# Kernel optimization log

Hardware: AMD Instinct MI355X
Metric: run time of the kernel (lower is better)

## Reference

```python
import jax, jax.numpy as jnp
import numpy as np

RADIUS = 5          # box-filter radius -> 11x11 kernel
TEMP = 0.5          # multinomial temperature
NSAMP = 5           # sampling_num
EPS = 1e-6
BN_EPS = 1e-5


def _conv(x, w, stride=1, padding=0, groups=1):
    return jax.lax.conv_general_dilated(
        x, w, window_strides=(stride, stride),
        padding=[(padding, padding), (padding, padding)],
        feature_group_count=groups,
        dimension_numbers=("NCHW", "OIHW", "NCHW"))


def custom_conv(x, w, key, stride=1, padding=0):
    """conv2d with cosine-activation regularization (bias=False path)."""
    B = x.shape[0]
    Cout = w.shape[0]
    # all-ones 'norm' conv on x*x
    x_norm = jnp.sqrt(_conv(x * x, jnp.ones_like(w), stride, padding))
    y = _conv(x, w, stride, padding)
    w_norm = jnp.sqrt(jnp.sum(w * w, axis=(1, 2, 3)))  # per-out-channel Frobenius norm
    cosine = y / (w_norm[None, :, None, None] + EPS) / (x_norm + EPS)
    # 11x11 depthwise box filter
    k = 2 * RADIUS + 1
    dw = jnp.ones((Cout, 1, k, k), x.dtype)
    cosine_mean = _conv(cosine, dw, 1, RADIUS, groups=Cout) / (k * k)
    H, W = cosine.shape[2], cosine.shape[3]
    # multinomial(NSAMP, exp(cosine/TEMP)) counts, no_grad in original
    logits = jax.lax.stop_gradient(cosine).reshape(B, Cout, H * W) / TEMP
    idx = jax.random.categorical(key, logits, axis=-1, shape=(NSAMP, B, Cout))
    bi = jnp.broadcast_to(jnp.arange(B)[None, :, None], (NSAMP, B, Cout))
    ci = jnp.broadcast_to(jnp.arange(Cout)[None, None, :], (NSAMP, B, Cout))
    mask = jnp.zeros((B, Cout, H * W), x.dtype).at[bi, ci, idx].add(1.0)
    cm = cosine_mean.reshape(B, Cout, H * W)
    act = ((mask * cm).sum(-1) / mask.sum(-1)).mean()
    return y, act


def batchnorm(x, g, b):
    # training-mode batch statistics (biased variance), like nn.BatchNorm2d
    m = x.mean(axis=(0, 2, 3), keepdims=True)
    v = x.var(axis=(0, 2, 3), keepdims=True)
    return (x - m) / jnp.sqrt(v + BN_EPS) * g[None, :, None, None] + b[None, :, None, None]


def setup_inputs() -> dict:
    key = jax.random.key(0)
    ks = jax.random.split(key, 10)
    x = jax.random.normal(ks[0], (16, 256, 56, 56), jnp.float32)
    w1 = jax.random.normal(ks[1], (64, 256, 1, 1), jnp.float32) * 0.05
    w2 = jax.random.normal(ks[2], (64, 64, 3, 3), jnp.float32) * 0.05
    w3 = jax.random.normal(ks[3], (256, 64, 1, 1), jnp.float32) * 0.05
    g1 = 1.0 + 0.05 * jax.random.normal(ks[4], (64,), jnp.float32)
    b1 = 0.05 * jax.random.normal(ks[5], (64,), jnp.float32)
    g2 = 1.0 + 0.05 * jax.random.normal(ks[6], (64,), jnp.float32)
    b2 = 0.05 * jax.random.normal(ks[7], (64,), jnp.float32)
    g3 = 1.0 + 0.05 * jax.random.normal(ks[8], (256,), jnp.float32)
    b3 = 0.05 * jax.random.normal(ks[9], (256,), jnp.float32)
    return {"x": x, "w1": w1, "w2": w2, "w3": w3,
            "g1": g1, "b1": b1, "g2": g2, "b2": b2, "g3": g3, "b3": b3}


def reference(x, w1, w2, w3, g1, b1, g2, b2, g3, b3):
    k0, k1, k2 = jax.random.split(jax.random.key(42), 3)
    acc = jnp.asarray(0.0, x.dtype)
    out, a = custom_conv(x, w1, k0)           # conv1x1
    acc = acc + a
    out = jax.nn.relu(batchnorm(out, g1, b1))
    out, a = custom_conv(out, w2, k1, padding=1)  # conv3x3, stride 1
    acc = acc + a
    out = jax.nn.relu(batchnorm(out, g2, b2))
    out, a = custom_conv(out, w3, k2)         # conv1x1 expand
    acc = acc + a
    out = batchnorm(out, g3, b3)
    out = jax.nn.relu(out + x)                # identity shortcut (downsample=None)
    return out, acc
```

## Files before the change

### kernel.cpp

```cpp
#include <hip/hip_runtime.h>
#include <stdint.h>
#include <math.h>

#define HW 3136
#define NPIX 50176

typedef __attribute__((ext_vector_type(8))) short bf16x8;
typedef __attribute__((ext_vector_type(4))) float f32x4;
#define MFMA16(a, b, c) __builtin_amdgcn_mfma_f32_16x16x32_bf16(a, b, c, 0, 0, 0)

__device__ __forceinline__ unsigned short f2bf(float f) {
  unsigned u = __float_as_uint(f);
  u = (u + 0x7fffu + ((u >> 16) & 1u)) >> 16;
  return (unsigned short)u;
}
__device__ __forceinline__ unsigned pk2(float a, float b) {
  return (unsigned)f2bf(a) | ((unsigned)f2bf(b) << 16);
}
__device__ __forceinline__ float bf2f(unsigned short h) {
  return __uint_as_float(((unsigned)h) << 16);
}

#define ROTL32(v, r) __builtin_rotateleft32((uint32_t)(v), (r))

__host__ __device__ inline void threefry2x32(uint32_t k0, uint32_t k1,
                                             uint32_t x0, uint32_t x1,
                                             uint32_t& o0, uint32_t& o1) {
  uint32_t k2 = k0 ^ k1 ^ 0x1BD11BDAu;
  x0 += k0; x1 += k1;
  x0 += x1; x1 = ROTL32(x1, 13); x1 ^= x0;
  x0 += x1; x1 = ROTL32(x1, 15); x1 ^= x0;
  x0 += x1; x1 = ROTL32(x1, 26); x1 ^= x0;
  x0 += x1; x1 = ROTL32(x1, 6);  x1 ^= x0;
  x0 += k1; x1 += k2 + 1u;
  x0 += x1; x1 = ROTL32(x1, 17); x1 ^= x0;
  x0 += x1; x1 = ROTL32(x1, 29); x1 ^= x0;
  x0 += x1; x1 = ROTL32(x1, 16); x1 ^= x0;
  x0 += x1; x1 = ROTL32(x1, 24); x1 ^= x0;
  x0 += k2; x1 += k0 + 2u;
  x0 += x1; x1 = ROTL32(x1, 13); x1 ^= x0;
  x0 += x1; x1 = ROTL32(x1, 15); x1 ^= x0;
  x0 += x1; x1 = ROTL32(x1, 26); x1 ^= x0;
  x0 += x1; x1 = ROTL32(x1, 6);  x1 ^= x0;
  x0 += k0; x1 += k1 + 3u;
  x0 += x1; x1 = ROTL32(x1, 17); x1 ^= x0;
  x0 += x1; x1 = ROTL32(x1, 29); x1 ^= x0;
  x0 += x1; x1 = ROTL32(x1, 16); x1 ^= x0;
  x0 += x1; x1 = ROTL32(x1, 24); x1 ^= x0;
  x0 += k1; x1 += k2 + 4u;
  x0 += x1; x1 = ROTL32(x1, 13); x1 ^= x0;
  x0 += x1; x1 = ROTL32(x1, 15); x1 ^= x0;
  x0 += x1; x1 = ROTL32(x1, 26); x1 ^= x0;
  x0 += x1; x1 = ROTL32(x1, 6);  x1 ^= x0;
  x0 += k2; x1 += k0 + 5u;
  o0 = x0; o1 = x1;
}

#define TF5_R(r)                                            \
  _Pragma("unroll") for (int i = 0; i < 5; ++i) {           \
    x0[i] += x1[i]; x1[i] = ROTL32(x1[i], r) ^ x0[i];       \
  }
#define TF5_INJ(a, b)                                       \
  _Pragma("unroll") for (int i = 0; i < 5; ++i) {           \
    x0[i] += (a); x1[i] += (b);                             \
  }
__device__ __forceinline__ void threefry5(uint32_t k0, uint32_t k1,
    const uint32_t xa[5], const uint32_t xb[5], uint32_t oa[5], uint32_t ob[5]) {
  uint32_t k2 = k0 ^ k1 ^ 0x1BD11BDAu;
  uint32_t x0[5], x1[5];
  #pragma unroll
  for (int i = 0; i < 5; ++i) { x0[i] = xa[i] + k0; x1[i] = xb[i] + k1; }
  TF5_R(13) TF5_R(15) TF5_R(26) TF5_R(6)  TF5_INJ(k1, k2 + 1u)
  TF5_R(17) TF5_R(29) TF5_R(16) TF5_R(24) TF5_INJ(k2, k0 + 2u)
  TF5_R(13) TF5_R(15) TF5_R(26) TF5_R(6)  TF5_INJ(k0, k1 + 3u)
  TF5_R(17) TF5_R(29) TF5_R(16) TF5_R(24) TF5_INJ(k1, k2 + 4u)
  TF5_R(13) TF5_R(15) TF5_R(26) TF5_R(6)  TF5_INJ(k2, k0 + 5u)
  #pragma unroll
  for (int i = 0; i < 5; ++i) { oa[i] = x0[i]; ob[i] = x1[i]; }
}

#define NLN2F -0.6931471805599453f
#define NEG2LOG2E -2.8853900817779268f
__device__ __forceinline__ float exp_draw(uint32_t bits) {
  float u = __uint_as_float((bits >> 9) | 0x3f800000u) - 1.0f;
  u = fmaxf(u, 1.17549435e-38f);
  return NLN2F * __log2f(u);
}

__global__ void wprep_k(const float* __restrict__ w1, const float* __restrict__ w2,
                        const float* __restrict__ w3, float* __restrict__ invwn,
                        unsigned short* __restrict__ W1b, unsigned short* __restrict__ W2tb,
                        unsigned short* __restrict__ W3b) {
  int i = blockIdx.x * 256 + threadIdx.x;
  if (i < 16384) {
    W1b[i] = f2bf(w1[i]);
  } else if (i < 53248) {
    int o = i - 16384;
    int co = o / 576, r = o % 576, tap = r >> 6, ci = r & 63;
    W2tb[o] = f2bf(w2[co * 576 + ci * 9 + tap]);
  } else if (i < 69632) {
    int o = i - 53248;
    W3b[o] = f2bf(w3[o]);
  } else {
    int t = i - 69632;
    if (t < 64) {
      float s = 0.f;
      for (int k = 0; k < 256; k++) { float v = w1[t * 256 + k]; s = fmaf(v, v, s); }
      invwn[t] = 1.0f / (sqrtf(s) + 1e-6f);
    } else if (t < 128) {
      int c = t - 64; float s = 0.f;
      for (int k = 0; k < 576; k++) { float v = w2[c * 576 + k]; s = fmaf(v, v, s); }
      invwn[t] = 1.0f / (sqrtf(s) + 1e-6f);
    } else if (t < 384) {
      int c = t - 128; float s = 0.f;
      for (int k = 0; k < 64; k++) { float v = w3[c * 64 + k]; s = fmaf(v, v, s); }
      invwn[t] = 1.0f / (sqrtf(s) + 1e-6f);
    }
  }
}

__global__ __launch_bounds__(256) void bn_fin(const float* __restrict__ Sp,
    const float* __restrict__ Qp, const float* __restrict__ g,
    const float* __restrict__ b, float* __restrict__ sc, float* __restrict__ sh,
    int nblk) {
  const int c = blockIdx.x, tid = threadIdx.x;
  const float* rs = Sp + (size_t)c * nblk;
  const float* rq = Qp + (size_t)c * nblk;
  float s = 0.f, q = 0.f;
  for (int i = tid; i < nblk; i += 256) { s += rs[i]; q += rq[i]; }
  #pragma unroll
  for (int o = 32; o; o >>= 1) { s += __shfl_xor(s, o); q += __shfl_xor(q, o); }
  __shared__ float S[4], Q[4];
  int lane = tid & 63, wave = tid >> 6;
  if (lane == 0) { S[wave] = s; Q[wave] = q; }
  __syncthreads();
  if (tid == 0) {
    float st = S[0] + S[1] + S[2] + S[3];
    float qt = Q[0] + Q[1] + Q[2] + Q[3];
    float mean = st * (1.0f / (float)NPIX);
    float var = qt * (1.0f / (float)NPIX) - mean * mean;
    float sv = g[c] / sqrtf(var + 1e-5f);
    sc[c] = sv; sh[c] = b[c] - mean * sv;
  }
}

__global__ __launch_bounds__(256) void conv1_mfma(
    const float* __restrict__ X, const unsigned short* __restrict__ Wb,
    const float* __restrict__ invwn, unsigned short* __restrict__ Y1,
    unsigned short* __restrict__ CS, float* __restrict__ Sp, float* __restrict__ Qp) {
#define ST1 264
#define NB1 784
  __shared__ __align__(16) unsigned short bq[64 * ST1];
  __shared__ float sqp[4][64];
  __shared__ float ixn[64];
  const int p0 = blockIdx.x * 64, b = blockIdx.y;
  const int bid = b * 49 + blockIdx.x;
  const int tid = threadIdx.x;
  const int lane = tid & 63, wave = tid >> 6;
  const int m = lane & 15, quad = lane >> 4;
  const int co0 = wave * 16;
  const float* Xb = X + (size_t)b * 256 * HW + p0;

  bf16x8 afr[8];
  const unsigned short* wrow = Wb + (co0 + m) * 256 + quad * 8;
  #pragma unroll
  for (int k = 0; k < 8; ++k) afr[k] = *(const bf16x8*)(wrow + k * 32);

  {
    const int px = tid & 63, rg = tid >> 6;
    float sq = 0.f;
    #pragma unroll
    for (int it = 0; it < 16; ++it) {
      int ci = rg * 64 + it * 4;
      float v0 = Xb[(size_t)(ci + 0) * HW + px];
      float v1 = Xb[(size_t)(ci + 1) * HW + px];
      float v2 = Xb[(size_t)(ci + 2) * HW + px];
      float v3 = Xb[(size_t)(ci + 3) * HW + px];
      sq += v0 * v0 + v1 * v1 + v2 * v2 + v3 * v3;
      *(uint2*)&bq[px * ST1 + ci] = make_uint2(pk2(v0, v1), pk2(v2, v3));
    }
    sqp[rg][px] = sq;
  }
  __syncthreads();
  if (tid < 64)
    ixn[tid] = 1.0f / (sqrtf(sqp[0][tid] + sqp[1][tid] + sqp[2][tid] + sqp[3][tid]) + 1e-6f);
  __syncthreads();

  f32x4 acc[4];
  #pragma unroll
  for (int nt = 0; nt < 4; ++nt) acc[nt] = (f32x4)0.f;
  #pragma unroll
  for (int nt = 0; nt < 4; ++nt) {
    const unsigned short* brow = &bq[(nt * 16 + m) * ST1 + quad * 8];
    #pragma unroll
    for (int k = 0; k < 8; ++k) {
      bf16x8 bfrag = *(const bf16x8*)(brow + k * 32);
      acc[nt] = MFMA16(afr[k], bfrag, acc[nt]);
    }
  }

  float s[4] = {0, 0, 0, 0}, q[4] = {0, 0, 0, 0};
  #pragma unroll
  for (int nt = 0; nt < 4; ++nt) {
    int px = nt * 16 + m;
    size_t bp = (size_t)b * HW + p0 + px;
    float ix = ixn[px];
    *(uint2*)&Y1[bp * 64 + co0 + quad * 4] =
        make_uint2(pk2(acc[nt][0], acc[nt][1]), pk2(acc[nt][2], acc[nt][3]));
    #pragma unroll
    for (int r = 0; r < 4; ++r) {
      int co = co0 + quad * 4 + r;
      float v = acc[nt][r];
      CS[((size_t)b * 64 + co) * HW + p0 + px] = f2bf(v * invwn[co] * ix);
      s[r] += v; q[r] = fmaf(v, v, q[r]);
    }
  }
  #pragma unroll
  for (int r = 0; r < 4; ++r) {
    float ss = s[r], qq = q[r];
    #pragma unroll
    for (int o = 8; o; o >>= 1) { ss += __shfl_xor(ss, o); qq += __shfl_xor(qq, o); }
    if (m == 0) {
      int co = co0 + quad * 4 + r;
      Sp[(size_t)co * NB1 + bid] = ss; Qp[(size_t)co * NB1 + bid] = qq;
    }
  }
#undef NB1
#undef ST1
}

__global__ __launch_bounds__(256) void chansum_px(const unsigned short* __restrict__ Y1,
    const float* __restrict__ sc, const float* __restrict__ sh,
    float* __restrict__ part) {
  int g = blockIdx.x * 256 + threadIdx.x;
  const unsigned short* row = Y1 + (size_t)g * 64;
  float s = 0.f;
  #pragma unroll
  for (int j = 0; j < 8; ++j) {
    uint4 d = *(const uint4*)(row + j * 8);
    unsigned dd[4] = {d.x, d.y, d.z, d.w};
    #pragma unroll
    for (int e = 0; e < 4; ++e) {
      int c = j * 8 + e * 2;
      float v0 = fmaxf(0.f, fmaf(bf2f((unsigned short)(dd[e] & 0xffff)), sc[c], sh[c]));
      float v1 = fmaxf(0.f, fmaf(bf2f((unsigned short)(dd[e] >> 16)), sc[c + 1], sh[c + 1]));
      s = fmaf(v0, v0, s); s = fmaf(v1, v1, s);
    }
  }
  part[g] = s;
}

__global__ __launch_bounds__(256) void box3inv(const float* __restrict__ part,
                                               float* __restrict__ out) {
  int g = blockIdx.x * 256 + threadIdx.x;
  int b = g / HW, p = g - b * HW;
  int y = p / 56, x = p % 56;
  float tot = 0.f;
  for (int dy = -1; dy <= 1; dy++) {
    int yy = y + dy; if (yy < 0 || yy >= 56) continue;
    for (int dx = -1; dx <= 1; dx++) {
      int xx = x + dx; if (xx < 0 || xx >= 56) continue;
      tot += part[b * HW + yy * 56 + xx];
    }
  }
  out[g] = 1.0f / (sqrtf(tot) + 1e-6f);
}

__global__ __launch_bounds__(256) void conv2_mfma(
    const unsigned short* __restrict__ Y1, const unsigned short* __restrict__ W2tb,
    const float* __restrict__ invwn, const float* __restrict__ ixn2,
    const float* __restrict__ sc1, const float* __restrict__ sh1,
    unsigned short* __restrict__ Y2, unsigned short* __restrict__ CS,
    float* __restrict__ Sp, float* __restrict__ Qp) {
#define STW 72
#define NB2 896
  __shared__ __align__(16) unsigned short ts[3 * 66 * STW];
  __shared__ float scl[64], shl[64];
  const int h = blockIdx.x, b = blockIdx.y;
  const int bid = b * 56 + h;
  const int tid = threadIdx.x;
  const int lane = tid & 63, wave = tid >> 6;
  const int m = lane & 15, quad = lane >> 4;
  const int co0 = wave * 16;
  if (tid < 64) { scl[tid] = sc1[tid]; shl[tid] = sh1[tid]; }

  bf16x8 afr[18];
  #pragma unroll
  for (int ks = 0; ks < 18; ++ks)
    afr[ks] = *(const bf16x8*)(W2tb + (co0 + m) * 576 + ks * 32 + quad * 8);
  __syncthreads();

  for (int l = tid; l < 6336; l += 256) {
    int cp = l & 31, cc = (l >> 5) % 66, dy = l / 2112;
    int yy = h - 1 + dy, xx = cc - 1;
    unsigned pkv = 0u;
    if (yy >= 0 && yy < 56 && xx >= 0 && xx < 56) {
      unsigned d = *(const unsigned*)&Y1[((size_t)b * HW + yy * 56 + xx) * 64 + cp * 2];
      float v0 = bf2f((unsigned short)(d & 0xffff));
      float v1 = bf2f((unsigned short)(d >> 16));
      v0 = fmaxf(0.f, fmaf(v0, scl[cp * 2], shl[cp * 2]));
      v1 = fmaxf(0.f, fmaf(v1, scl[cp * 2 + 1], shl[cp * 2 + 1]));
      pkv = pk2(v0, v1);
    }
    *(unsigned*)&ts[(dy * 66 + cc) * STW + cp * 2] = pkv;
  }
  __syncthreads();

  f32x4 acc[4];
  #pragma unroll
  for (int nt = 0; nt < 4; ++nt) acc[nt] = (f32x4)0.f;
  #pragma unroll
  for (int nt = 0; nt < 4; ++nt) {
    #pragma unroll
    for (int ks = 0; ks < 18; ++ks) {
      int tap = ks >> 1, half = ks & 1;
      int dy = tap / 3, dx = tap % 3;
      bf16x8 bfrag = *(const bf16x8*)&ts[(dy * 66 + nt * 16 + m + dx) * STW + half * 32 + quad * 8];
      acc[nt] = MFMA16(afr[ks], bfrag, acc[nt]);
    }
  }

  float s[4] = {0, 0, 0, 0}, q[4] = {0, 0, 0, 0};
  #pragma unroll
  for (int nt = 0; nt < 4; ++nt) {
    int px = nt * 16 + m;
    bool valid = px < 56;
    int pix = h * 56 + px;
    if (valid) {
      float ix = ixn2[b * HW + pix];
      size_t bp = (size_t)b * HW + pix;
      *(uint2*)&Y2[bp * 64 + co0 + quad * 4] =
          make_uint2(pk2(acc[nt][0], acc[nt][1]), pk2(acc[nt][2], acc[nt][3]));
      #pragma unroll
      for (int r = 0; r < 4; ++r) {
        int co = co0 + quad * 4 + r;
        CS[((size_t)b * 64 + co) * HW + pix] = f2bf(acc[nt][r] * invwn[co] * ix);
      }
    }
    #pragma unroll
    for (int r = 0; r < 4; ++r) {
      float v = valid ? acc[nt][r] : 0.f;
      s[r] += v; q[r] = fmaf(v, v, q[r]);
    }
  }
  #pragma unroll
  for (int r = 0; r < 4; ++r) {
    float ss = s[r], qq = q[r];
    #pragma unroll
    for (int o = 8; o; o >>= 1) { ss += __shfl_xor(ss, o); qq += __shfl_xor(qq, o); }
    if (m == 0) {
      int co = co0 + quad * 4 + r;
      Sp[(size_t)co * NB2 + bid] = ss; Qp[(size_t)co * NB2 + bid] = qq;
    }
  }
#undef NB2
#undef STW
}

__global__ __launch_bounds__(256) void conv3_mfma(
    const unsigned short* __restrict__ Y2, const unsigned short* __restrict__ W3b,
    const float* __restrict__ invwn,
    const float* __restrict__ sc2, const float* __restrict__ sh2,
    unsigned short* __restrict__ Y3, unsigned short* __restrict__ CS,
    float* __restrict__ Sp, float* __restrict__ Qp) {
#define ST3 72
#define NB3 784
  __shared__ __align__(16) unsigned short bq[64 * ST3];
  __shared__ float scl[64], shl[64], sqp[4][64], ixn[64];
  const int p0 = blockIdx.x * 64, b = blockIdx.y;
  const int bid = b * 49 + blockIdx.x;
  const int tid = threadIdx.x;
  const int lane = tid & 63, wave = tid >> 6;
  const int m = lane & 15, quad = lane >> 4;
  const int co0 = wave * 64;
  if (tid < 64) { scl[tid] = sc2[tid]; shl[tid] = sh2[tid]; }

  bf16x8 afr[4][2];
  #pragma unroll
  for (int mt = 0; mt < 4; ++mt)
    #pragma unroll
    for (int k = 0; k < 2; ++k)
      afr[mt][k] = *(const bf16x8*)(W3b + (co0 + mt * 16 + m) * 64 + k * 32 + quad * 8);
  __syncthreads();

  {
    const int cp = tid & 31, pxg = tid >> 5;
    #pragma unroll
    for (int it = 0; it < 8; ++it) {
      int px = pxg * 8 + it;
      unsigned d = *(const unsigned*)&Y2[((size_t)b * HW + p0 + px) * 64 + cp * 2];
      float v0 = bf2f((unsigned short)(d & 0xffff));
      float v1 = bf2f((unsigned short)(d >> 16));
      v0 = fmaxf(0.f, fmaf(v0, scl[cp * 2], shl[cp * 2]));
      v1 = fmaxf(0.f, fmaf(v1, scl[cp * 2 + 1], shl[cp * 2 + 1]));
      *(unsigned*)&bq[px * ST3 + cp * 2] = pk2(v0, v1);
    }
  }
  __syncthreads();
  {
    const int px = tid & 63, hh = tid >> 6;
    const unsigned short* row = &bq[px * ST3 + hh * 16];
    float sq = 0.f;
    #pragma unroll
    for (int e = 0; e < 16; ++e) { float v = bf2f(row[e]); sq = fmaf(v, v, sq); }
    sqp[hh][px] = sq;
  }
  __syncthreads();
  if (tid < 64)
    ixn[tid] = 1.0f / (sqrtf(sqp[0][tid] + sqp[1][tid] + sqp[2][tid] + sqp[3][tid]) + 1e-6f);
  __syncthreads();

  f32x4 acc[4][4];
  #pragma unroll
  for (int mt = 0; mt < 4; ++mt)
    #pragma unroll
    for (int nt = 0; nt < 4; ++nt) acc[mt][nt] = (f32x4)0.f;
  #pragma unroll
  for (int nt = 0; nt < 4; ++nt) {
    const unsigned short* brow = &bq[(nt * 16 + m) * ST3 + quad * 8];
    bf16x8 b0 = *(const bf16x8*)(brow);
    bf16x8 b1 = *(const bf16x8*)(brow + 32);
    #pragma unroll
    for (int mt = 0; mt < 4; ++mt) {
      acc[mt][nt] = MFMA16(afr[mt][0], b0, acc[mt][nt]);
      acc[mt][nt] = MFMA16(afr[mt][1], b1, acc[mt][nt]);
    }
  }

  #pragma unroll
  for (int mt = 0; mt < 4; ++mt) {
    float s[4] = {0, 0, 0, 0}, q[4] = {0, 0, 0, 0};
    #pragma unroll
    for (int nt = 0; nt < 4; ++nt) {
      int px = nt * 16 + m;
      float ix = ixn[px];
      #pragma unroll
      for (int r = 0; r < 4; ++r) {
        int co = co0 + mt * 16 + quad * 4 + r;
        float v = acc[mt][nt][r];
        size_t off = ((size_t)b * 256 + co) * HW + p0 + px;
        Y3[off] = f2bf(v);
        CS[off] = f2bf(v * invwn[co] * ix);
        s[r] += v; q[r] = fmaf(v, v, q[r]);
      }
    }
    #pragma unroll
    for (int r = 0; r < 4; ++r) {
      float ss = s[r], qq = q[r];
      #pragma unroll
      for (int o = 8; o; o >>= 1) { ss += __shfl_xor(ss, o); qq += __shfl_xor(qq, o); }
      if (m == 0) {
        int co = co0 + mt * 16 + quad * 4 + r;
        Sp[(size_t)co * NB3 + bid] = ss; Qp[(size_t)co * NB3 + bid] = qq;
      }
    }
  }
#undef NB3
#undef ST3
}

template <int NT>
__global__ __launch_bounds__(NT) void sample5_k(const unsigned short* __restrict__ CS,
    float* __restrict__ acc, uint32_t key0, uint32_t key1, int BC, float scale) {
  const int u = blockIdx.x;
  const int v = u + (BC >> 1);
  const uint32_t sC = (uint32_t)BC * (uint32_t)HW;
  const uint32_t halfn = sC * 2u + (sC >> 1);
  const unsigned short* rowU = CS + (size_t)u * HW;
  const unsigned short* rowV = CS + (size_t)v * HW;
  const int tid = threadIdx.x;
  const int lane = tid & 63;

  __shared__ unsigned kmin[10];
  __shared__ float wsum[10];
  if (tid < 10) { kmin[tid] = 0xFFFFFFFFu; wsum[tid] = 0.f; }

  unsigned bk[10];
  #pragma unroll
  for (int k = 0; k < 10; ++k) bk[k] = 0xFFFFFFFFu;

  const uint32_t baseU0 = (uint32_t)u * (uint32_t)HW;
  const uint32_t baseV0 = (uint32_t)v * (uint32_t)HW;
  for (int p = tid; p < HW; p += NT) {
    float wu = __builtin_amdgcn_exp2f(bf2f(rowU[p]) * NEG2LOG2E);
    float wv = __builtin_amdgcn_exp2f(bf2f(rowV[p]) * NEG2LOG2E);
    uint32_t eU = baseU0 + (uint32_t)p;
    uint32_t eV = baseV0 + (uint32_t)p;
    uint32_t xa[5] = {eU, eU + sC, eU + 2 * sC, eV, eV + sC};
    uint32_t xb[5] = {eU + halfn, eU + sC + halfn, eU + 2 * sC + halfn,
                      eV + halfn, eV + sC + halfn};
    uint32_t oa[5], ob[5];
    threefry5(key0, key1, xa, xb, oa, ob);
    uint32_t wds[10] = {oa[0], oa[1], oa[2], ob[3], ob[4],
                        oa[3], oa[4], ob[0], ob[1], ob[2]};
    #pragma unroll
    for (int k = 0; k < 10; ++k) {
      float s = exp_draw(wds[k]) * (k < 5 ? wu : wv);
      unsigned key = (__float_as_uint(s) & 0xFFFFF000u) | (unsigned)p;
      bk[k] = bk[k] < key ? bk[k] : key;
    }
  }

  __syncthreads();
  #pragma unroll
  for (int k = 0; k < 10; ++k) {
    unsigned kv = bk[k];
    #pragma unroll
    for (int o = 32; o; o >>= 1) {
      unsigned ov = __shfl_xor(kv, o);
      kv = kv < ov ? kv : ov;
    }
    if (lane == 0) atomicMin(&kmin[k], kv);
  }
  __syncthreads();

  for (int idx = tid; idx < 1210; idx += NT) {
    int win = idx / 121, j = idx - win * 121;
    int bidx = (int)(kmin[win] & 0xFFFu);
    int py = bidx / 56, px = bidx % 56;
    int yy = py + j / 11 - 5, xx = px + j % 11 - 5;
    if (yy >= 0 && yy < 56 && xx >= 0 && xx < 56) {
      const unsigned short* row = (win < 5) ? rowU : rowV;
      atomicAdd(&wsum[win], bf2f(row[yy * 56 + xx]));
    }
  }
  __syncthreads();
  if (tid == 0) {
    float t = 0.f;
    #pragma unroll
    for (int k = 0; k < 10; ++k) t += wsum[k];
    atomicAdd(acc, t * scale);
  }
}

__global__ __launch_bounds__(256) void final_k(const unsigned short* __restrict__ Y3,
    const float* __restrict__ X, const float* __restrict__ sc,
    const float* __restrict__ sh, const float* __restrict__ acc,
    float* __restrict__ out) {
  size_t i4 = (size_t)blockIdx.x * 256 + threadIdx.x;
  if (i4 == 0) out[12845056] = acc[0];
  size_t i = i4 * 4;
  int c = (int)((i / HW) % 256);
  float a = sc[c], d = sh[c];
  uint2 yd = *(const uint2*)&Y3[i];
  float4 xv = *(const float4*)&X[i];
  float4 r;
  r.x = fmaxf(0.f, fmaf(bf2f((unsigned short)(yd.x & 0xffff)), a, d) + xv.x);
  r.y = fmaxf(0.f, fmaf(bf2f((unsigned short)(yd.x >> 16)),    a, d) + xv.y);
  r.z = fmaxf(0.f, fmaf(bf2f((unsigned short)(yd.y & 0xffff)), a, d) + xv.z);
  r.w = fmaxf(0.f, fmaf(bf2f((unsigned short)(yd.y >> 16)),    a, d) + xv.w);
  *(float4*)&out[i] = r;
}

extern "C" void kernel_launch(void* const* d_in, const int* in_sizes, int n_in,
                              void* d_out, int out_size, void* d_ws, size_t ws_size,
                              hipStream_t stream) {
  (void)in_sizes; (void)n_in; (void)out_size; (void)ws_size;
  const float* x  = (const float*)d_in[0];
  const float* w1 = (const float*)d_in[1];
  const float* w2 = (const float*)d_in[2];
  const float* w3 = (const float*)d_in[3];
  const float* g1 = (const float*)d_in[4];
  const float* b1 = (const float*)d_in[5];
  const float* g2 = (const float*)d_in[6];
  const float* b2 = (const float*)d_in[7];
  const float* g3 = (const float*)d_in[8];
  const float* b3 = (const float*)d_in[9];
  float* out = (float*)d_out;
  float* ws = (float*)d_ws;

  size_t o = 0;
  unsigned short* y3b  = (unsigned short*)(ws + o); o += 6422528;
  unsigned short* cos3 = (unsigned short*)(ws + o); o += 6422528;
  unsigned short* CSb  = (unsigned short*)(ws + o); o += 1605632;
  unsigned short* y1b  = (unsigned short*)(ws + o); o += 1605632;
  unsigned short* y2b  = (unsigned short*)(ws + o); o += 1605632;
  unsigned short* W1b  = (unsigned short*)(ws + o); o += 8192;
  unsigned short* W2tb = (unsigned short*)(ws + o); o += 18432;
  unsigned short* W3b  = (unsigned short*)(ws + o); o += 8192;
  float* part = ws + o; o += NPIX;
  float* ixn2 = ws + o; o += NPIX;
  float* invwn = ws + o; o += 384;
  float* Sp1 = ws + o; o += 64 * 784;   float* Qp1 = ws + o; o += 64 * 784;
  float* Sp2 = ws + o; o += 64 * 896;   float* Qp2 = ws + o; o += 64 * 896;
  float* Sp3 = ws + o; o += 256 * 784;  float* Qp3 = ws + o; o += 256 * 784;
  float* acc = ws + o; o += 1;
  float* sc1 = ws + o; o += 64;  float* sh1 = ws + o; o += 64;
  float* sc2 = ws + o; o += 64;  float* sh2 = ws + o; o += 64;
  float* sc3 = ws + o; o += 256; float* sh3 = ws + o; o += 256;

  hipMemsetAsync(acc, 0, sizeof(float), stream);

  uint32_t A0, B0, A1, B1, A2, B2;
  threefry2x32(0u, 42u, 0u, 3u, A0, B0);
  threefry2x32(0u, 42u, 1u, 4u, A1, B1);
  threefry2x32(0u, 42u, 2u, 5u, A2, B2);

  const float scale64  = 1.0f / (121.0f * 5.0f * 1024.0f);
  const float scale256 = 1.0f / (121.0f * 5.0f * 4096.0f);

  wprep_k<<<274, 256, 0, stream>>>(w1, w2, w3, invwn, W1b, W2tb, W3b);

  conv1_mfma<<<dim3(49, 16), 256, 0, stream>>>(x, W1b, invwn, y1b, CSb, Sp1, Qp1);
  bn_fin<<<64, 256, 0, stream>>>(Sp1, Qp1, g1, b1, sc1, sh1, 784);
  sample5_k<512><<<512, 512, 0, stream>>>(CSb, acc, A0, A1, 1024, scale64);

  chansum_px<<<196, 256, 0, stream>>>(y1b, sc1, sh1, part);
  box3inv<<<196, 256, 0, stream>>>(part, ixn2);
  conv2_mfma<<<dim3(56, 16), 256, 0, stream>>>(
      y1b, W2tb, invwn + 64, ixn2, sc1, sh1, y2b, CSb, Sp2, Qp2);
  bn_fin<<<64, 256, 0, stream>>>(Sp2, Qp2, g2, b2, sc2, sh2, 896);
  sample5_k<512><<<512, 512, 0, stream>>>(CSb, acc, A2, B0, 1024, scale64);

  conv3_mfma<<<dim3(49, 16), 256, 0, stream>>>(
      y2b, W3b, invwn + 128, sc2, sh2, y3b, cos3, Sp3, Qp3);
  bn_fin<<<256, 256, 0, stream>>>(Sp3, Qp3, g3, b3, sc3, sh3, 784);
  sample5_k<256><<<2048, 256, 0, stream>>>(cos3, acc, B1, B2, 4096, scale256);
  final_k<<<12544, 256, 0, stream>>>(y3b, x, sc3, sh3, acc, out);
}
```

Baseline: 382.3 us.

## Split sampling kernel across five sample blocks per row pair

The sampling kernel used to compute all five threefry draws for both rows of a pair inside one block. Now a second grid dimension gives each sample index its own block, and each thread computes a single threefry2x32 per pixel, covering one U-draw and one V-draw. This raises parallelism and cuts per-thread register pressure. In exchange, each row is read and exp-weighted five times instead of once, and there are more blocks and more global atomics.

```diff
diff --git a/kernel.cpp b/kernel.cpp
--- a/kernel.cpp
+++ b/kernel.cpp
@@ -56,29 +56,6 @@
   o0 = x0; o1 = x1;
 }
 
-#define TF5_R(r)                                            \
-  _Pragma("unroll") for (int i = 0; i < 5; ++i) {           \
-    x0[i] += x1[i]; x1[i] = ROTL32(x1[i], r) ^ x0[i];       \
-  }
-#define TF5_INJ(a, b)                                       \
-  _Pragma("unroll") for (int i = 0; i < 5; ++i) {           \
-    x0[i] += (a); x1[i] += (b);                             \
-  }
-__device__ __forceinline__ void threefry5(uint32_t k0, uint32_t k1,
-    const uint32_t xa[5], const uint32_t xb[5], uint32_t oa[5], uint32_t ob[5]) {
-  uint32_t k2 = k0 ^ k1 ^ 0x1BD11BDAu;
-  uint32_t x0[5], x1[5];
-  #pragma unroll
-  for (int i = 0; i < 5; ++i) { x0[i] = xa[i] + k0; x1[i] = xb[i] + k1; }
-  TF5_R(13) TF5_R(15) TF5_R(26) TF5_R(6)  TF5_INJ(k1, k2 + 1u)
-  TF5_R(17) TF5_R(29) TF5_R(16) TF5_R(24) TF5_INJ(k2, k0 + 2u)
-  TF5_R(13) TF5_R(15) TF5_R(26) TF5_R(6)  TF5_INJ(k0, k1 + 3u)
-  TF5_R(17) TF5_R(29) TF5_R(16) TF5_R(24) TF5_INJ(k1, k2 + 4u)
-  TF5_R(13) TF5_R(15) TF5_R(26) TF5_R(6)  TF5_INJ(k2, k0 + 5u)
-  #pragma unroll
-  for (int i = 0; i < 5; ++i) { oa[i] = x0[i]; ob[i] = x1[i]; }
-}
-
 #define NLN2F -0.6931471805599453f
 #define NEG2LOG2E -2.8853900817779268f
 __device__ __forceinline__ float exp_draw(uint32_t bits) {
@@ -459,10 +436,10 @@
 #undef ST3
 }
 
-template <int NT>
-__global__ __launch_bounds__(NT) void sample5_k(const unsigned short* __restrict__ CS,
+__global__ __launch_bounds__(256) void sample_k(const unsigned short* __restrict__ CS,
     float* __restrict__ acc, uint32_t key0, uint32_t key1, int BC, float scale) {
   const int u = blockIdx.x;
+  const int k = blockIdx.y;
   const int v = u + (BC >> 1);
   const uint32_t sC = (uint32_t)BC * (uint32_t)HW;
   const uint32_t halfn = sC * 2u + (sC >> 1);
@@ -470,67 +447,54 @@
   const unsigned short* rowV = CS + (size_t)v * HW;
   const int tid = threadIdx.x;
   const int lane = tid & 63;
-
-  __shared__ unsigned kmin[10];
-  __shared__ float wsum[10];
-  if (tid < 10) { kmin[tid] = 0xFFFFFFFFu; wsum[tid] = 0.f; }
-
-  unsigned bk[10];
-  #pragma unroll
-  for (int k = 0; k < 10; ++k) bk[k] = 0xFFFFFFFFu;
-
-  const uint32_t baseU0 = (uint32_t)u * (uint32_t)HW;
-  const uint32_t baseV0 = (uint32_t)v * (uint32_t)HW;
-  for (int p = tid; p < HW; p += NT) {
+  const bool o0isU = (k < 3);
+  const uint32_t base = o0isU ? ((uint32_t)u * HW + (uint32_t)k * sC)
+                              : ((uint32_t)v * HW + (uint32_t)(k - 3) * sC);
+
+  __shared__ unsigned kmin[2];
+  __shared__ float wsum[2];
+  if (tid < 2) { kmin[tid] = 0xFFFFFFFFu; wsum[tid] = 0.f; }
+
+  unsigned bkU = 0xFFFFFFFFu, bkV = 0xFFFFFFFFu;
+  for (int p = tid; p < HW; p += 256) {
     float wu = __builtin_amdgcn_exp2f(bf2f(rowU[p]) * NEG2LOG2E);
     float wv = __builtin_amdgcn_exp2f(bf2f(rowV[p]) * NEG2LOG2E);
-    uint32_t eU = baseU0 + (uint32_t)p;
-    uint32_t eV = baseV0 + (uint32_t)p;
-    uint32_t xa[5] = {eU, eU + sC, eU + 2 * sC, eV, eV + sC};
-    uint32_t xb[5] = {eU + halfn, eU + sC + halfn, eU + 2 * sC + halfn,
-                      eV + halfn, eV + sC + halfn};
-    uint32_t oa[5], ob[5];
-    threefry5(key0, key1, xa, xb, oa, ob);
-    uint32_t wds[10] = {oa[0], oa[1], oa[2], ob[3], ob[4],
-                        oa[3], oa[4], ob[0], ob[1], ob[2]};
-    #pragma unroll
-    for (int k = 0; k < 10; ++k) {
-      float s = exp_draw(wds[k]) * (k < 5 ? wu : wv);
-      unsigned key = (__float_as_uint(s) & 0xFFFFF000u) | (unsigned)p;
-      bk[k] = bk[k] < key ? bk[k] : key;
-    }
-  }
-
-  __syncthreads();
-  #pragma unroll
-  for (int k = 0; k < 10; ++k) {
-    unsigned kv = bk[k];
-    #pragma unroll
-    for (int o = 32; o; o >>= 1) {
-      unsigned ov = __shfl_xor(kv, o);
-      kv = kv < ov ? kv : ov;
-    }
-    if (lane == 0) atomicMin(&kmin[k], kv);
-  }
-  __syncthreads();
-
-  for (int idx = tid; idx < 1210; idx += NT) {
+    uint32_t e = base + (uint32_t)p;
+    uint32_t o0, o1;
+    threefry2x32(key0, key1, e, e + halfn, o0, o1);
+    uint32_t wU = o0isU ? o0 : o1;
+    uint32_t wV = o0isU ? o1 : o0;
+    float sU = exp_draw(wU) * wu;
+    float sV = exp_draw(wV) * wv;
+    unsigned keyU = (__float_as_uint(sU) & 0xFFFFF000u) | (unsigned)p;
+    unsigned keyV = (__float_as_uint(sV) & 0xFFFFF000u) | (unsigned)p;
+    bkU = bkU < keyU ? bkU : keyU;
+    bkV = bkV < keyV ? bkV : keyV;
+  }
+
+  __syncthreads();
+  #pragma unroll
+  for (int o = 32; o; o >>= 1) {
+    unsigned oU = __shfl_xor(bkU, o);
+    unsigned oV = __shfl_xor(bkV, o);
+    bkU = bkU < oU ? bkU : oU;
+    bkV = bkV < oV ? bkV : oV;
+  }
+  if (lane == 0) { atomicMin(&kmin[0], bkU); atomicMin(&kmin[1], bkV); }
+  __syncthreads();
+
+  for (int idx = tid; idx < 242; idx += 256) {
     int win = idx / 121, j = idx - win * 121;
     int bidx = (int)(kmin[win] & 0xFFFu);
     int py = bidx / 56, px = bidx % 56;
     int yy = py + j / 11 - 5, xx = px + j % 11 - 5;
     if (yy >= 0 && yy < 56 && xx >= 0 && xx < 56) {
-      const unsigned short* row = (win < 5) ? rowU : rowV;
+      const unsigned short* row = win ? rowV : rowU;
       atomicAdd(&wsum[win], bf2f(row[yy * 56 + xx]));
     }
   }
   __syncthreads();
-  if (tid == 0) {
-    float t = 0.f;
-    #pragma unroll
-    for (int k = 0; k < 10; ++k) t += wsum[k];
-    atomicAdd(acc, t * scale);
-  }
+  if (tid == 0) atomicAdd(acc, (wsum[0] + wsum[1]) * scale);
 }
 
 __global__ __launch_bounds__(256) void final_k(const unsigned short* __restrict__ Y3,
@@ -603,18 +567,18 @@
 
   conv1_mfma<<<dim3(49, 16), 256, 0, stream>>>(x, W1b, invwn, y1b, CSb, Sp1, Qp1);
   bn_fin<<<64, 256, 0, stream>>>(Sp1, Qp1, g1, b1, sc1, sh1, 784);
-  sample5_k<512><<<512, 512, 0, stream>>>(CSb, acc, A0, A1, 1024, scale64);
+  sample_k<<<dim3(512, 5), 256, 0, stream>>>(CSb, acc, A0, A1, 1024, scale64);
 
   chansum_px<<<196, 256, 0, stream>>>(y1b, sc1, sh1, part);
   box3inv<<<196, 256, 0, stream>>>(part, ixn2);
   conv2_mfma<<<dim3(56, 16), 256, 0, stream>>>(
       y1b, W2tb, invwn + 64, ixn2, sc1, sh1, y2b, CSb, Sp2, Qp2);
   bn_fin<<<64, 256, 0, stream>>>(Sp2, Qp2, g2, b2, sc2, sh2, 896);
-  sample5_k<512><<<512, 512, 0, stream>>>(CSb, acc, A2, B0, 1024, scale64);
+  sample_k<<<dim3(512, 5), 256, 0, stream>>>(CSb, acc, A2, B0, 1024, scale64);
 
   conv3_mfma<<<dim3(49, 16), 256, 0, stream>>>(
       y2b, W3b, invwn + 128, sc2, sh2, y3b, cos3, Sp3, Qp3);
   bn_fin<<<256, 256, 0, stream>>>(Sp3, Qp3, g3, b3, sc3, sh3, 784);
-  sample5_k<256><<<2048, 256, 0, stream>>>(cos3, acc, B1, B2, 4096, scale256);
+  sample_k<<<dim3(2048, 5), 256, 0, stream>>>(cos3, acc, B1, B2, 4096, scale256);
   final_k<<<12544, 256, 0, stream>>>(y3b, x, sc3, sh3, acc, out);
 }
```

Result: slower. 434.4 us (+13.6%).
